# Optimization experiments

Hardware: AMD Instinct MI355X
Metric: run time of the kernel (lower is better)

The kernel has to match this reference:

```python
import jax, jax.numpy as jnp
import numpy as np

NUM_HEADS = 16
NUM_KV_HEADS = 4
HEAD_DIM = 128
DIM = 2048
B, S = 2, 2048


def apply_rotary(t, cos, sin):
    # t: [B, S, H, D]; cos/sin: [S, D//2] -> broadcast [1, S, 1, D//2]
    tr = t.reshape(*t.shape[:-1], HEAD_DIM // 2, 2)
    t_r, t_i = tr[..., 0], tr[..., 1]
    c = cos[None, :, None, :]
    s = sin[None, :, None, :]
    o_r = t_r * c - t_i * s
    o_i = t_r * s + t_i * c
    return jnp.stack([o_r, o_i], axis=-1).reshape(t.shape)


def setup_inputs() -> dict:
    key = jax.random.key(0)
    ks = jax.random.split(key, 7)
    sc = 1.0 / np.sqrt(DIM)
    x = jax.random.normal(ks[0], (B, S, DIM), jnp.float32)
    pos = jnp.arange(S, dtype=jnp.float32)[:, None]
    inv_freq = 1.0 / (10000.0 ** (jnp.arange(0, HEAD_DIM, 2, dtype=jnp.float32) / HEAD_DIM))
    ang = pos * inv_freq[None, :]
    freqs_cos = jnp.cos(ang)
    freqs_sin = jnp.sin(ang)
    w_q = jax.random.normal(ks[1], (DIM, NUM_HEADS * HEAD_DIM), jnp.float32) * sc
    w_k = jax.random.normal(ks[2], (DIM, NUM_KV_HEADS * HEAD_DIM), jnp.float32) * sc
    w_v = jax.random.normal(ks[3], (DIM, NUM_KV_HEADS * HEAD_DIM), jnp.float32) * sc
    w_o = jax.random.normal(ks[4], (NUM_HEADS * HEAD_DIM, DIM), jnp.float32) * sc
    return {"x": x, "freqs_cos": freqs_cos, "freqs_sin": freqs_sin,
            "w_q": w_q, "w_k": w_k, "w_v": w_v, "w_o": w_o}


def reference(x, freqs_cos, freqs_sin, w_q, w_k, w_v, w_o):
    b, s, _ = x.shape
    kv_rep = NUM_HEADS // NUM_KV_HEADS
    q = (x @ w_q).reshape(b, s, NUM_HEADS, HEAD_DIM)
    k = (x @ w_k).reshape(b, s, NUM_KV_HEADS, HEAD_DIM)
    v = (x @ w_v).reshape(b, s, NUM_KV_HEADS, HEAD_DIM)
    q = apply_rotary(q, freqs_cos, freqs_sin)
    k = apply_rotary(k, freqs_cos, freqs_sin)
    # GQA: repeat KV heads to match query heads
    k = jnp.repeat(k, kv_rep, axis=2)
    v = jnp.repeat(v, kv_rep, axis=2)
    scores = jnp.einsum('bqhd,bkhd->bhqk', q, k) / np.sqrt(HEAD_DIM)
    causal = jnp.triu(jnp.full((s, s), -jnp.inf, jnp.float32), k=1)
    scores = scores + causal[None, None, :, :]
    attn = jax.nn.softmax(scores, axis=-1)
    out = jnp.einsum('bhqk,bkhd->bqhd', attn, v).reshape(b, s, NUM_HEADS * HEAD_DIM)
    return out @ w_o
```

## Files before the change

### kernel.cpp

```cpp
#include <hip/hip_runtime.h>
#include <stdint.h>

#define DIMSZ 2048
#define NH 16
#define NKV 4
#define HD 128
#define BATCH 2
#define SEQ 2048
#define MROWS (BATCH*SEQ)
#define NQKV (NH*HD + 2*NKV*HD)

typedef unsigned short u16;
typedef float f32x4 __attribute__((ext_vector_type(4)));
typedef short short8 __attribute__((ext_vector_type(8)));
typedef __bf16 bf16x8 __attribute__((ext_vector_type(8)));
typedef unsigned short u16x4 __attribute__((ext_vector_type(4)));

__device__ __forceinline__ u16 f2bf(float f) {
  __bf16 h = (__bf16)f;
  return __builtin_bit_cast(u16, h);
}

__device__ __forceinline__ float bf2f(u16 h) {
  union { uint32_t u; float f; } v; v.u = ((uint32_t)h) << 16; return v.f;
}

__device__ __forceinline__ void async16(void* lds, const void* g) {
  __builtin_amdgcn_global_load_lds(
      (const __attribute__((address_space(1))) void*)(g),
      (__attribute__((address_space(3))) void*)(lds), 16, 0, 0);
}

__device__ __forceinline__ bf16x8 load_frag(const u16* p) {
  short8 v = *reinterpret_cast<const short8*>(p);
  return __builtin_bit_cast(bf16x8, v);
}

__global__ void cast_x_kernel(const float* __restrict__ x, u16* __restrict__ xb) {
  int i = (blockIdx.x * blockDim.x + threadIdx.x) * 4;
  float4 v = *reinterpret_cast<const float4*>(x + i);
  u16x4 o;
  o.x = f2bf(v.x); o.y = f2bf(v.y); o.z = f2bf(v.z); o.w = f2bf(v.w);
  *reinterpret_cast<u16x4*>(xb + i) = o;
}

__global__ __launch_bounds__(1024) void wtrans_all_kernel(const float* __restrict__ wq,
                                                          const float* __restrict__ wk,
                                                          const float* __restrict__ wv,
                                                          const float* __restrict__ wo,
                                                          u16* __restrict__ wtqkv,
                                                          u16* __restrict__ wto) {
  __shared__ float t[32][33];
  int y = blockIdx.y;
  const float* src; int srcN; u16* dst; int nbase;
  if (y < 64)      { src = wq; srcN = 2048; dst = wtqkv;                          nbase = y * 32; }
  else if (y < 80) { src = wk; srcN = 512;  dst = wtqkv + (size_t)2048 * 2048;    nbase = (y - 64) * 32; }
  else if (y < 96) { src = wv; srcN = 512;  dst = wtqkv + (size_t)2560 * 2048;    nbase = (y - 80) * 32; }
  else             { src = wo; srcN = 2048; dst = wto;                            nbase = (y - 96) * 32; }
  int k0 = blockIdx.x * 32;
  int tx = threadIdx.x, ty = threadIdx.y;
  t[ty][tx] = src[(size_t)(k0 + ty) * srcN + nbase + tx];
  __syncthreads();
  dst[(size_t)(nbase + ty) * 2048 + k0 + tx] = f2bf(t[tx][ty]);
}

#define COMPUTE_PAIR(q)                                                              \
  {                                                                                  \
    bf16x8 af[2][2];                                                                 \
    _Pragma("unroll")                                                                \
    for (int m2 = 0; m2 < 2; ++m2)                                                   \
      _Pragma("unroll")                                                              \
      for (int kk = 0; kk < 2; ++kk)                                                 \
        af[m2][kk] = load_frag(&lds[buf][0][wm * 8192 +                              \
            (((q) * 2 + m2) * 16 + l16) * 64 + ((kk * 4 + lg) ^ (l16 & 7)) * 8]);    \
    __builtin_amdgcn_s_setprio(1);                                                   \
    _Pragma("unroll")                                                                \
    for (int m2 = 0; m2 < 2; ++m2)                                                   \
      _Pragma("unroll")                                                              \
      for (int ni = 0; ni < 4; ++ni)                                                 \
        _Pragma("unroll")                                                            \
        for (int kk = 0; kk < 2; ++kk)                                               \
          acc[(q) * 2 + m2][ni] = __builtin_amdgcn_mfma_f32_16x16x32_bf16(           \
              af[m2][kk], bper[ni][kk], acc[(q) * 2 + m2][ni], 0, 0, 0);             \
    __builtin_amdgcn_s_setprio(0);                                                   \
  }

template <bool BF16OUT>
__global__ __launch_bounds__(512, 2) void gemm8p_kernel(const u16* __restrict__ A,
                                                        const u16* __restrict__ BT,
                                                        void* __restrict__ Cp,
                                                        int M, int N, int K, int gx) {
  __shared__ u16 lds[2][2][16384];
  const int tid = threadIdx.x;
  const int wave = tid >> 6, lane = tid & 63;
  const int l16 = lane & 15, lg = lane >> 4;
  const int wm = wave >> 2, wn = wave & 3;
  const int rloc = lane >> 3;
  const int sOff = ((lane & 7) ^ rloc) * 8;
  const int nwg = gridDim.x;
  const int swz = (blockIdx.x & 7) * (nwg >> 3) + (blockIdx.x >> 3);
  const int bm = (swz / gx) * 256, bn = (swz % gx) * 256;

  f32x4 acc[8][4] = {};

  auto stage = [&](int dstbuf, int x, int h, const u16* xp, int xr0, int kk0) {
#pragma unroll
    for (int j = 0; j < 2; ++j) {
      int c = j * 8 + wave;
      async16(&lds[dstbuf][x][h * 8192 + c * 512],
              xp + (size_t)(xr0 + h * 128 + c * 8 + rloc) * K + kk0 + sOff);
    }
  };

  stage(0, 0, 0, A, bm, 0);
  stage(0, 0, 1, A, bm, 0);
  stage(0, 1, 0, BT, bn, 0);
  stage(0, 1, 1, BT, bn, 0);

  const int NT = K >> 6;
  for (int kt = 0; kt < NT; ++kt) {
    const int buf = kt & 1, nbuf = buf ^ 1;
    const int k0n = (kt + 1) << 6;
    const bool pf = (kt + 1 < NT);
    bf16x8 bper[4][2];

    if (pf) {
      stage(nbuf, 0, 0, A, bm, k0n);
      asm volatile("s_waitcnt vmcnt(2)" ::: "memory");
    } else {
      asm volatile("s_waitcnt vmcnt(0)" ::: "memory");
    }
    __builtin_amdgcn_s_barrier();
    __builtin_amdgcn_sched_barrier(0);
#pragma unroll
    for (int ni = 0; ni < 4; ++ni)
#pragma unroll
      for (int kk = 0; kk < 2; ++kk)
        bper[ni][kk] = load_frag(&lds[buf][1][(wn >> 1) * 8192 +
            ((wn & 1) * 64 + ni * 16 + l16) * 64 + ((kk * 4 + lg) ^ (l16 & 7)) * 8]);
    COMPUTE_PAIR(0)
    if (pf) stage(nbuf, 0, 1, A, bm, k0n);
    __builtin_amdgcn_s_barrier();
    __builtin_amdgcn_sched_barrier(0);
    COMPUTE_PAIR(1)
    if (pf) stage(nbuf, 1, 0, BT, bn, k0n);
    __builtin_amdgcn_s_barrier();
    __builtin_amdgcn_sched_barrier(0);
    COMPUTE_PAIR(2)
    if (pf) stage(nbuf, 1, 1, BT, bn, k0n);
    __builtin_amdgcn_s_barrier();
    __builtin_amdgcn_sched_barrier(0);
    COMPUTE_PAIR(3)
    __builtin_amdgcn_s_barrier();
  }

#pragma unroll
  for (int mi = 0; mi < 8; ++mi)
#pragma unroll
    for (int ni = 0; ni < 4; ++ni)
#pragma unroll
      for (int r = 0; r < 4; ++r) {
        size_t idx = (size_t)(bm + wm * 128 + mi * 16 + lg * 4 + r) * N +
                     bn + wn * 64 + ni * 16 + l16;
        if (BF16OUT) ((u16*)Cp)[idx] = f2bf(acc[mi][ni][r]);
        else         ((float*)Cp)[idx] = acc[mi][ni][r];
      }
}

#define COMPUTE_MB(q)                                                                \
  {                                                                                  \
    bf16x8 af[2];                                                                    \
    _Pragma("unroll")                                                                \
    for (int kk = 0; kk < 2; ++kk)                                                   \
      af[kk] = load_frag(&lds2[buf][(wm * 64 + (q) * 16 + l16) * 64 +                \
                                    ((kk * 4 + lg) ^ (l16 & 7)) * 8]);               \
    __builtin_amdgcn_s_setprio(1);                                                   \
    _Pragma("unroll")                                                                \
    for (int ni = 0; ni < 4; ++ni)                                                   \
      _Pragma("unroll")                                                              \
      for (int kk = 0; kk < 2; ++kk)                                                 \
        acc[(q)][ni] = __builtin_amdgcn_mfma_f32_16x16x32_bf16(                      \
            af[kk], bper[ni][kk], acc[(q)][ni], 0, 0, 0);                            \
    __builtin_amdgcn_s_setprio(0);                                                   \
  }

__global__ __launch_bounds__(512, 2) void gemm8p_n128_kernel(const u16* __restrict__ A,
                                                             const u16* __restrict__ BT,
                                                             float* __restrict__ C,
                                                             int M, int N, int K, int gx) {
  __shared__ u16 lds2[2][24576];
  const int tid = threadIdx.x;
  const int wave = tid >> 6, lane = tid & 63;
  const int l16 = lane & 15, lg = lane >> 4;
  const int wm = wave >> 1, wn = wave & 1;
  const int rloc = lane >> 3;
  const int sOff = ((lane & 7) ^ rloc) * 8;
  const int nwg = gridDim.x;
  const int swz = (blockIdx.x & 7) * (nwg >> 3) + (blockIdx.x >> 3);
  const int bm = (swz / gx) * 256, bn = (swz % gx) * 128;

  f32x4 acc[4][4] = {};

  auto stageA = [&](int dstbuf, int h, int kk0) {
#pragma unroll
    for (int j = 0; j < 2; ++j) {
      int c = j * 8 + wave;
      async16(&lds2[dstbuf][h * 8192 + c * 512],
              A + (size_t)(bm + h * 128 + c * 8 + rloc) * K + kk0 + sOff);
    }
  };
  auto stageB = [&](int dstbuf, int kk0) {
#pragma unroll
    for (int j = 0; j < 2; ++j) {
      int c = j * 8 + wave;
      async16(&lds2[dstbuf][16384 + c * 512],
              BT + (size_t)(bn + c * 8 + rloc) * K + kk0 + sOff);
    }
  };

  stageA(0, 0, 0);
  stageA(0, 1, 0);
  stageB(0, 0);

  const int NT = K >> 6;
  for (int kt = 0; kt < NT; ++kt) {
    const int buf = kt & 1, nbuf = buf ^ 1;
    const int k0n = (kt + 1) << 6;
    const bool pf = (kt + 1 < NT);
    bf16x8 bper[4][2];

    if (pf) {
      stageA(nbuf, 0, k0n);
      asm volatile("s_waitcnt vmcnt(2)" ::: "memory");
    } else {
      asm volatile("s_waitcnt vmcnt(0)" ::: "memory");
    }
    __builtin_amdgcn_s_barrier();
    __builtin_amdgcn_sched_barrier(0);
#pragma unroll
    for (int ni = 0; ni < 4; ++ni)
#pragma unroll
      for (int kk = 0; kk < 2; ++kk)
        bper[ni][kk] = load_frag(&lds2[buf][16384 +
            (wn * 64 + ni * 16 + l16) * 64 + ((kk * 4 + lg) ^ (l16 & 7)) * 8]);
    COMPUTE_MB(0)
    if (pf) stageA(nbuf, 1, k0n);
    __builtin_amdgcn_s_barrier();
    __builtin_amdgcn_sched_barrier(0);
    COMPUTE_MB(1)
    if (pf) stageB(nbuf, k0n);
    __builtin_amdgcn_s_barrier();
    __builtin_amdgcn_sched_barrier(0);
    COMPUTE_MB(2)
    __builtin_amdgcn_s_barrier();
    __builtin_amdgcn_sched_barrier(0);
    COMPUTE_MB(3)
    __builtin_amdgcn_s_barrier();
  }

#pragma unroll
  for (int mb = 0; mb < 4; ++mb)
#pragma unroll
    for (int ni = 0; ni < 4; ++ni)
#pragma unroll
      for (int r = 0; r < 4; ++r)
        C[(size_t)(bm + wm * 64 + mb * 16 + lg * 4 + r) * N +
          bn + wn * 64 + ni * 16 + l16] = acc[mb][ni][r];
}

__global__ void rope_k_kernel(const u16* __restrict__ qkv, const float* __restrict__ fc,
                              const float* __restrict__ fs, u16* __restrict__ Kb) {
  int gi = blockIdx.x * blockDim.x + threadIdx.x;
  int i = gi & 63;
  int t = gi >> 6;
  int s = t & (SEQ - 1), b = t >> 11;
  int kh = blockIdx.y;
  float c = fc[s * 64 + i], sn = fs[s * 64 + i];
  uint32_t pr = *reinterpret_cast<const uint32_t*>(&qkv[(size_t)t * NQKV + NH * HD + kh * HD + 2 * i]);
  float tr = bf2f((u16)(pr & 0xffff)), ti = bf2f((u16)(pr >> 16));
  uint32_t w = (uint32_t)f2bf(tr * c - ti * sn) |
               ((uint32_t)f2bf(tr * sn + ti * c) << 16);
  *reinterpret_cast<uint32_t*>(&Kb[((size_t)(b * NKV + kh) * SEQ + s) * HD + 2 * i]) = w;
}

__global__ __launch_bounds__(1024) void vtrans_kernel(const u16* __restrict__ qkv,
                                                      u16* __restrict__ vt) {
  __shared__ u16 t[32][33];
  int s0 = blockIdx.x * 32, d0 = blockIdx.y * 32;
  int bk = blockIdx.z;
  int b = bk >> 2, kh = bk & 3;
  int tx = threadIdx.x, ty = threadIdx.y;
  t[ty][tx] = qkv[(size_t)(b * SEQ + s0 + ty) * NQKV + NH * HD + NKV * HD + kh * HD + d0 + tx];
  __syncthreads();
  vt[((size_t)(b * NKV + kh) * HD + d0 + ty) * SEQ + s0 + tx] = t[tx][ty];
}

__global__ __launch_bounds__(256) void attn_kernel(const u16* __restrict__ qkv,
                                                   const float* __restrict__ fc,
                                                   const float* __restrict__ fs,
                                                   const u16* __restrict__ Kc,
                                                   const u16* __restrict__ VT,
                                                   u16* __restrict__ AO) {
  __shared__ u16 Ks[2][64 * 128];
  __shared__ u16 Vs[2][128 * 64];
  __shared__ u16 Ps[4][16 * 64];
  const int pairi = blockIdx.x;
  const int h = blockIdx.y, b = blockIdx.z;
  const int kvh = h >> 2;
  const int tid = threadIdx.x, wave = tid >> 6, lane = tid & 63;
  const int l16 = lane & 15, lg = lane >> 4;

  const u16* Kbase = Kc + (size_t)(b * NKV + kvh) * SEQ * HD;
  const u16* Vbase = VT + (size_t)(b * NKV + kvh) * HD * SEQ;

  bf16x8 onesf;
#pragma unroll
  for (int j = 0; j < 8; ++j) onesf[j] = __builtin_bit_cast(__bf16, (u16)0x3F80);

  int kOff[4], vOff[4], kDst[4], vDst[4];
#pragma unroll
  for (int i = 0; i < 4; ++i) {
    int chunk = i * 4 + wave;
    int krow = chunk * 4 + (lane >> 4);
    kOff[i] = krow * HD + ((lane & 15) ^ (krow & 15)) * 8;
    kDst[i] = chunk * 512;
    int vrow = chunk * 8 + (lane >> 3);
    vOff[i] = vrow * SEQ + ((lane & 7) ^ (vrow & 7)) * 8;
    vDst[i] = chunk * 512;
  }

  for (int sel = 0; sel < 2; ++sel) {
    const int qblk = sel ? pairi : (31 - pairi);
    const int qrow0 = qblk * 64 + wave * 16;
    const int rq = qrow0 + l16;

    const float qs = 0.12751689760098266f;
    const u16* Qrow = qkv + (size_t)(b * SEQ + rq) * NQKV + h * HD;
    const float* fcb = fc + (size_t)rq * 64;
    const float* fsb = fs + (size_t)rq * 64;
    bf16x8 qf[4];
#pragma unroll
    for (int c = 0; c < 4; ++c) {
      bf16x8 raw = load_frag(Qrow + c * 32 + lg * 8);
      float4 cc = *reinterpret_cast<const float4*>(fcb + c * 16 + lg * 4);
      float4 sv = *reinterpret_cast<const float4*>(fsb + c * 16 + lg * 4);
      bf16x8 q;
#pragma unroll
      for (int j = 0; j < 4; ++j) {
        float e = (float)raw[2 * j], od = (float)raw[2 * j + 1];
        float ce = (&cc.x)[j] * qs, se = (&sv.x)[j] * qs;
        q[2 * j]     = (__bf16)(e * ce - od * se);
        q[2 * j + 1] = (__bf16)(e * se + od * ce);
      }
      qf[c] = q;
    }

    f32x4 o[8] = {};
    f32x4 lsum = {};
    float m = -3e38f;

    __syncthreads();
#pragma unroll
    for (int i = 0; i < 4; ++i) {
      async16(&Ks[0][kDst[i]], Kbase + kOff[i]);
      async16(&Vs[0][vDst[i]], Vbase + vOff[i]);
    }

    for (int kt = 0; kt <= qblk; ++kt) {
      const int cur = kt & 1;
      __syncthreads();
      if (kt < qblk) {
        const int k0n = (kt + 1) * 64;
#pragma unroll
        for (int i = 0; i < 4; ++i) {
          async16(&Ks[cur ^ 1][kDst[i]], Kbase + (size_t)k0n * HD + kOff[i]);
          async16(&Vs[cur ^ 1][vDst[i]], Vbase + k0n + vOff[i]);
        }
      }

      f32x4 s[4] = {};
      __builtin_amdgcn_s_setprio(1);
#pragma unroll
      for (int cb = 0; cb < 4; ++cb) {
#pragma unroll
        for (int c = 0; c < 4; ++c) {
          bf16x8 kf = load_frag(&Ks[cur][(cb * 16 + l16) * 128 + (((c * 4 + lg) ^ l16) & 15) * 8]);
          s[cb] = __builtin_amdgcn_mfma_f32_16x16x32_bf16(kf, qf[c], s[cb], 0, 0, 0);
        }
      }
      __builtin_amdgcn_s_setprio(0);

      if (kt == qblk) {
        const int k0 = kt * 64;
#pragma unroll
        for (int cb = 0; cb < 4; ++cb) {
#pragma unroll
          for (int r = 0; r < 4; ++r) {
            int key = k0 + cb * 16 + lg * 4 + r;
            if (key > rq) s[cb][r] = -1e30f;
          }
        }
      }

      float v0 = fmaxf(fmaxf(fmaxf(s[0][0], s[0][1]), fmaxf(s[0][2], s[0][3])),
                       fmaxf(fmaxf(s[1][0], s[1][1]), fmaxf(s[1][2], s[1][3])));
      v0 = fmaxf(v0, fmaxf(fmaxf(fmaxf(s[2][0], s[2][1]), fmaxf(s[2][2], s[2][3])),
                           fmaxf(fmaxf(s[3][0], s[3][1]), fmaxf(s[3][2], s[3][3]))));
      v0 = fmaxf(v0, __shfl_xor(v0, 16));
      v0 = fmaxf(v0, __shfl_xor(v0, 32));

      bool need = v0 > m + 8.f;
      if (__any(need)) {
        float newm = fmaxf(m, v0);
        float sc = exp2f(m - newm);
        m = newm;
        float scR[4];
#pragma unroll
        for (int r = 0; r < 4; ++r) scR[r] = __shfl(sc, lg * 4 + r);
#pragma unroll
        for (int r = 0; r < 4; ++r) {
          lsum[r] *= scR[r];
#pragma unroll
          for (int db = 0; db < 8; ++db) o[db][r] *= scR[r];
        }
      }

#pragma unroll
      for (int cb = 0; cb < 4; ++cb) {
        uint32_t lo = (uint32_t)f2bf(exp2f(s[cb][0] - m)) |
                      ((uint32_t)f2bf(exp2f(s[cb][1] - m)) << 16);
        uint32_t hi = (uint32_t)f2bf(exp2f(s[cb][2] - m)) |
                      ((uint32_t)f2bf(exp2f(s[cb][3] - m)) << 16);
        int idx = (l16 * 64 + cb * 16 + lg * 4) ^ ((l16 & 7) << 3);
        uint64_t w = (uint64_t)lo | ((uint64_t)hi << 32);
        *reinterpret_cast<uint64_t*>(&Ps[wave][idx]) = w;
      }

      bf16x8 pf[2];
#pragma unroll
      for (int c = 0; c < 2; ++c)
        pf[c] = load_frag(&Ps[wave][(l16 * 64 + c * 32 + lg * 8) ^ ((l16 & 7) << 3)]);
      __builtin_amdgcn_s_setprio(1);
#pragma unroll
      for (int c = 0; c < 2; ++c)
        lsum = __builtin_amdgcn_mfma_f32_16x16x32_bf16(pf[c], onesf, lsum, 0, 0, 0);
#pragma unroll
      for (int db = 0; db < 8; ++db) {
#pragma unroll
        for (int c = 0; c < 2; ++c) {
          bf16x8 vf = load_frag(&Vs[cur][(db * 16 + l16) * 64 + ((c * 4 + lg) ^ (l16 & 7)) * 8]);
          o[db] = __builtin_amdgcn_mfma_f32_16x16x32_bf16(pf[c], vf, o[db], 0, 0, 0);
        }
      }
      __builtin_amdgcn_s_setprio(0);
    }

#pragma unroll
    for (int r = 0; r < 4; ++r) {
      float inv = 1.f / lsum[r];
      int rqo = qrow0 + lg * 4 + r;
      size_t dst = ((size_t)(b * SEQ + rqo) * NH + h) * HD;
#pragma unroll
      for (int db = 0; db < 8; ++db)
        AO[dst + db * 16 + l16] = f2bf(o[db][r] * inv);
    }
  }
}

extern "C" void kernel_launch(void* const* d_in, const int* in_sizes, int n_in,
                              void* d_out, int out_size, void* d_ws, size_t ws_size,
                              hipStream_t stream) {
  (void)in_sizes; (void)n_in; (void)out_size; (void)ws_size;
  const float* x  = (const float*)d_in[0];
  const float* fc = (const float*)d_in[1];
  const float* fs = (const float*)d_in[2];
  const float* wq = (const float*)d_in[3];
  const float* wk = (const float*)d_in[4];
  const float* wv = (const float*)d_in[5];
  const float* wo = (const float*)d_in[6];
  float* out = (float*)d_out;

  char* ws = (char*)d_ws;
  u16*  xb    = (u16*)(ws);
  u16*  wtqkv = (u16*)(ws + 16777216);
  u16*  wto   = (u16*)(ws + 29360128);
  u16*  qkv   = (u16*)(ws + 37748736);
  u16*  Kb    = (u16*)(ws + 62914560);
  u16*  VTb   = (u16*)(ws + 67108864);
  u16*  AOb   = (u16*)(ws + 71303168);

  cast_x_kernel<<<dim3(8192), dim3(256), 0, stream>>>(x, xb);
  wtrans_all_kernel<<<dim3(64, 160), dim3(32, 32), 0, stream>>>(wq, wk, wv, wo, wtqkv, wto);

  gemm8p_kernel<true><<<dim3(192), dim3(512), 0, stream>>>(xb, wtqkv, qkv, MROWS, NQKV, DIMSZ, 12);

  rope_k_kernel<<<dim3(1024, 4), dim3(256), 0, stream>>>(qkv, fc, fs, Kb);
  vtrans_kernel<<<dim3(64, 4, 8), dim3(32, 32), 0, stream>>>(qkv, VTb);

  attn_kernel<<<dim3(16, 16, 2), dim3(256), 0, stream>>>(qkv, fc, fs, Kb, VTb, AOb);

  gemm8p_n128_kernel<<<dim3(256), dim3(512), 0, stream>>>(AOb, wto, out, MROWS, DIMSZ, DIMSZ, 16);
}
```

Measured before the change: 206.8 us.

## Software-pipeline attention loop so QK^T of next tile overlaps softmax of current

Restructures the flash-attention inner loop so the score MFMAs for key tile kt+1 are issued before the softmax/exp and PV MFMAs of tile kt, with K staged two tiles ahead and V one tile ahead. The goal is to hide exp/softmax VALU latency behind matrix-core work and to separate K and V prefetch timing. It holds an extra set of score registers live, which raises register pressure and may hurt occupancy, and it moves the barrier to the end of each iteration.

Result: slower. 244.0 us (+18.0%).

```diff
diff --git a/kernel.cpp b/kernel.cpp
--- a/kernel.cpp
+++ b/kernel.cpp
@@ -329,6 +329,19 @@
     vDst[i] = chunk * 512;
   }
 
+  auto stageK = [&](int j) {
+    const u16* base = Kbase + (size_t)(j * 64) * HD;
+    u16* dst = Ks[j & 1];
+#pragma unroll
+    for (int i = 0; i < 4; ++i) async16(&dst[kDst[i]], base + kOff[i]);
+  };
+  auto stageV = [&](int j) {
+    const u16* base = Vbase + j * 64;
+    u16* dst = Vs[j & 1];
+#pragma unroll
+    for (int i = 0; i < 4; ++i) async16(&dst[vDst[i]], base + vOff[i]);
+  };
+
   for (int sel = 0; sel < 2; ++sel) {
     const int qblk = sel ? pairi : (31 - pairi);
     const int qrow0 = qblk * 64 + wave * 16;
@@ -355,57 +368,58 @@
       qf[c] = q;
     }
 
+    auto qkt = [&](f32x4* sx, const u16* Kbuf) {
+      __builtin_amdgcn_s_setprio(1);
+#pragma unroll
+      for (int cb = 0; cb < 4; ++cb) {
+#pragma unroll
+        for (int c = 0; c < 4; ++c) {
+          bf16x8 kf = load_frag(&Kbuf[(cb * 16 + l16) * 128 + (((c * 4 + lg) ^ l16) & 15) * 8]);
+          sx[cb] = __builtin_amdgcn_mfma_f32_16x16x32_bf16(kf, qf[c], sx[cb], 0, 0, 0);
+        }
+      }
+      __builtin_amdgcn_s_setprio(0);
+    };
+    auto maskdiag = [&](f32x4* sx, int k0) {
+#pragma unroll
+      for (int cb = 0; cb < 4; ++cb)
+#pragma unroll
+        for (int r = 0; r < 4; ++r) {
+          int key = k0 + cb * 16 + lg * 4 + r;
+          if (key > rq) sx[cb][r] = -1e30f;
+        }
+    };
+
     f32x4 o[8] = {};
     f32x4 lsum = {};
     float m = -3e38f;
 
     __syncthreads();
-#pragma unroll
-    for (int i = 0; i < 4; ++i) {
-      async16(&Ks[0][kDst[i]], Kbase + kOff[i]);
-      async16(&Vs[0][vDst[i]], Vbase + vOff[i]);
-    }
+    stageK(0);
+    stageV(0);
+    if (qblk >= 1) stageK(1);
+    __syncthreads();
+
+    f32x4 sprev[4] = {};
+    qkt(sprev, Ks[0]);
+    if (qblk == 0) maskdiag(sprev, 0);
+    __syncthreads();
 
     for (int kt = 0; kt <= qblk; ++kt) {
-      const int cur = kt & 1;
-      __syncthreads();
-      if (kt < qblk) {
-        const int k0n = (kt + 1) * 64;
-#pragma unroll
-        for (int i = 0; i < 4; ++i) {
-          async16(&Ks[cur ^ 1][kDst[i]], Kbase + (size_t)k0n * HD + kOff[i]);
-          async16(&Vs[cur ^ 1][vDst[i]], Vbase + k0n + vOff[i]);
-        }
-      }
-
-      f32x4 s[4] = {};
-      __builtin_amdgcn_s_setprio(1);
-#pragma unroll
-      for (int cb = 0; cb < 4; ++cb) {
-#pragma unroll
-        for (int c = 0; c < 4; ++c) {
-          bf16x8 kf = load_frag(&Ks[cur][(cb * 16 + l16) * 128 + (((c * 4 + lg) ^ l16) & 15) * 8]);
-          s[cb] = __builtin_amdgcn_mfma_f32_16x16x32_bf16(kf, qf[c], s[cb], 0, 0, 0);
-        }
-      }
-      __builtin_amdgcn_s_setprio(0);
-
-      if (kt == qblk) {
-        const int k0 = kt * 64;
-#pragma unroll
-        for (int cb = 0; cb < 4; ++cb) {
-#pragma unroll
-          for (int r = 0; r < 4; ++r) {
-            int key = k0 + cb * 16 + lg * 4 + r;
-            if (key > rq) s[cb][r] = -1e30f;
-          }
-        }
-      }
-
-      float v0 = fmaxf(fmaxf(fmaxf(s[0][0], s[0][1]), fmaxf(s[0][2], s[0][3])),
-                       fmaxf(fmaxf(s[1][0], s[1][1]), fmaxf(s[1][2], s[1][3])));
-      v0 = fmaxf(v0, fmaxf(fmaxf(fmaxf(s[2][0], s[2][1]), fmaxf(s[2][2], s[2][3])),
-                           fmaxf(fmaxf(s[3][0], s[3][1]), fmaxf(s[3][2], s[3][3]))));
+      if (kt + 1 <= qblk) stageV(kt + 1);
+      if (kt + 2 <= qblk) stageK(kt + 2);
+
+      f32x4 scur[4] = {};
+      const bool havenext = kt < qblk;
+      if (havenext) {
+        qkt(scur, Ks[(kt + 1) & 1]);
+        if (kt + 1 == qblk) maskdiag(scur, (kt + 1) * 64);
+      }
+
+      float v0 = fmaxf(fmaxf(fmaxf(sprev[0][0], sprev[0][1]), fmaxf(sprev[0][2], sprev[0][3])),
+                       fmaxf(fmaxf(sprev[1][0], sprev[1][1]), fmaxf(sprev[1][2], sprev[1][3])));
+      v0 = fmaxf(v0, fmaxf(fmaxf(fmaxf(sprev[2][0], sprev[2][1]), fmaxf(sprev[2][2], sprev[2][3])),
+                           fmaxf(fmaxf(sprev[3][0], sprev[3][1]), fmaxf(sprev[3][2], sprev[3][3]))));
       v0 = fmaxf(v0, __shfl_xor(v0, 16));
       v0 = fmaxf(v0, __shfl_xor(v0, 32));
 
@@ -427,10 +441,10 @@
 
 #pragma unroll
       for (int cb = 0; cb < 4; ++cb) {
-        uint32_t lo = (uint32_t)f2bf(exp2f(s[cb][0] - m)) |
-                      ((uint32_t)f2bf(exp2f(s[cb][1] - m)) << 16);
-        uint32_t hi = (uint32_t)f2bf(exp2f(s[cb][2] - m)) |
-                      ((uint32_t)f2bf(exp2f(s[cb][3] - m)) << 16);
+        uint32_t lo = (uint32_t)f2bf(exp2f(sprev[cb][0] - m)) |
+                      ((uint32_t)f2bf(exp2f(sprev[cb][1] - m)) << 16);
+        uint32_t hi = (uint32_t)f2bf(exp2f(sprev[cb][2] - m)) |
+                      ((uint32_t)f2bf(exp2f(sprev[cb][3] - m)) << 16);
         int idx = (l16 * 64 + cb * 16 + lg * 4) ^ ((l16 & 7) << 3);
         uint64_t w = (uint64_t)lo | ((uint64_t)hi << 32);
         *reinterpret_cast<uint64_t*>(&Ps[wave][idx]) = w;
@@ -444,15 +458,22 @@
 #pragma unroll
       for (int c = 0; c < 2; ++c)
         lsum = __builtin_amdgcn_mfma_f32_16x16x32_bf16(pf[c], onesf, lsum, 0, 0, 0);
+      const u16* Vbuf = Vs[kt & 1];
 #pragma unroll
       for (int db = 0; db < 8; ++db) {
 #pragma unroll
         for (int c = 0; c < 2; ++c) {
-          bf16x8 vf = load_frag(&Vs[cur][(db * 16 + l16) * 64 + ((c * 4 + lg) ^ (l16 & 7)) * 8]);
+          bf16x8 vf = load_frag(&Vbuf[(db * 16 + l16) * 64 + ((c * 4 + lg) ^ (l16 & 7)) * 8]);
           o[db] = __builtin_amdgcn_mfma_f32_16x16x32_bf16(pf[c], vf, o[db], 0, 0, 0);
         }
       }
       __builtin_amdgcn_s_setprio(0);
+
+      if (havenext) {
+#pragma unroll
+        for (int cb = 0; cb < 4; ++cb) sprev[cb] = scur[cb];
+      }
+      __syncthreads();
     }
 
 #pragma unroll
```
